# Kernel optimization log

Hardware: AMD Instinct MI355X
Metric: run time of the kernel (lower is better)

## Reference

```python
import jax, jax.numpy as jnp
import numpy as np

B, T, MED, LAB, GLU, D = 1024, 25, 145, 1956, 16, 64
H = D // 2  # 32


def _gat(h, adj, w, a):
    # h: [B, MED, 1] drug-usage counts; in_features=1 so Wh = h * w
    Wh = h * w  # [B, MED, D]
    f1 = Wh @ a[:D]  # [B, MED]
    f2 = Wh @ a[D:]  # [B, MED]
    e = jax.nn.leaky_relu(f1[:, :, None] + f2[:, None, :], 0.2)  # [B, MED, MED]
    e = jnp.where(adj > 0, e, jnp.float32(-9e15))
    attn = jax.nn.softmax(e, axis=-1)
    return jax.nn.elu(attn @ Wh)  # [B, MED, D]


def _mha(q, k, v, wq, wk, wv, wo, nh=4):
    Bq, Lq, Dm = q.shape
    dh = Dm // nh
    qh = (q @ wq).reshape(Bq, Lq, nh, dh)
    kh = (k @ wk).reshape(Bq, k.shape[1], nh, dh)
    vh = (v @ wv).reshape(Bq, v.shape[1], nh, dh)
    s = jnp.einsum('bqhd,bkhd->bhqk', qh, kh) / np.float32(np.sqrt(dh))
    a = jax.nn.softmax(s, axis=-1)
    o = jnp.einsum('bhqk,bkhd->bqhd', a, vh).reshape(Bq, Lq, Dm)
    return o @ wo


def _gated(x, g):
    # Attn_encoder: per-position gated emphasis, preserves sequence shape
    return x * jax.nn.sigmoid(x @ g)[..., None]


def setup_inputs():
    key = jax.random.key(0)
    ks = jax.random.split(key, 40)
    n = lambda i, shape, s=0.05: (jax.random.normal(ks[i], shape, dtype=jnp.float32) * s)
    inp = {
        'lab': jax.random.normal(ks[0], (B, LAB), dtype=jnp.float32),
        'glu': jax.random.normal(ks[1], (B, T, GLU), dtype=jnp.float32),
        'time_feat': jax.random.uniform(ks[2], (B, T, GLU), dtype=jnp.float32),
        'med': jax.random.uniform(ks[3], (B, T, MED), dtype=jnp.float32),
        'ehr_adj': (jax.random.uniform(ks[4], (MED, MED)) > 0.9).astype(jnp.float32),
        'ddi_adj': (jax.random.uniform(ks[5], (MED, MED)) > 0.9).astype(jnp.float32),
        'time_adj': (jax.random.uniform(ks[6], (MED, MED)) > 0.9).astype(jnp.float32),
        'sll_w1': n(7, (LAB, D)), 'sll_b1': n(8, (D,)),
        'sll_w2': n(9, (D, H)), 'sll_b2': n(10, (H,)),
        'glu_w': n(11, (2 * GLU, H)), 'glu_b': n(12, (H,)), 'glu_gate': n(13, (H,)),
        'med_w': n(14, (MED, D)), 'med_b': n(15, (D,)), 'med_gate': n(16, (D,)),
        'gat_ehr_w': n(17, (D,)), 'gat_ehr_a': n(18, (2 * D,)),
        'gat_time_w': n(19, (D,)), 'gat_time_a': n(20, (2 * D,)),
        'gat_ddi_w': n(21, (D,)), 'gat_ddi_a': n(22, (2 * D,)),
        'ga_wq': n(23, (D, D)), 'ga_wk': n(24, (D, D)), 'ga_wv': n(25, (D, D)), 'ga_wo': n(26, (D, D)),
        'm1_wq': n(27, (D, D)), 'm1_wk': n(28, (D, D)), 'm1_wv': n(29, (D, D)), 'm1_wo': n(30, (D, D)),
        'm2_wq': n(31, (D, D)), 'm2_wk': n(32, (D, D)), 'm2_wv': n(33, (D, D)), 'm2_wo': n(34, (D, D)),
        'out_w1': n(35, (MED * D, MED * D // 8), 0.01), 'out_b1': n(36, (MED * D // 8,)),
        'out_w2': n(37, (MED * D // 8, MED)), 'out_b2': n(38, (MED,)),
    }
    return inp


def reference(lab, glu, time_feat, med, ehr_adj, ddi_adj, time_adj,
              sll_w1, sll_b1, sll_w2, sll_b2,
              glu_w, glu_b, glu_gate, med_w, med_b, med_gate,
              gat_ehr_w, gat_ehr_a, gat_time_w, gat_time_a, gat_ddi_w, gat_ddi_a,
              ga_wq, ga_wk, ga_wv, ga_wo,
              m1_wq, m1_wk, m1_wv, m1_wo,
              m2_wq, m2_wk, m2_wv, m2_wo,
              out_w1, out_b1, out_w2, out_b2):
    relu = jax.nn.relu
    medb = (med > 0.9).astype(med.dtype)  # multi-hot medication history
    # static_ll, repeated over visits
    static = relu(relu(lab @ sll_w1 + sll_b1) @ sll_w2 + sll_b2)  # [B, H]
    static_seq = jnp.broadcast_to(static[:, None, :], (B, T, H))
    # per-patient drug usage counts over past visits
    h = jnp.sum(medb[:, :-1], axis=1)[..., None]  # [B, MED, 1]
    g_ehr = _gat(h, ehr_adj, gat_ehr_w, gat_ehr_a)
    g_time = _gat(h, time_adj, gat_time_w, gat_time_a)
    g_ddi = _gat(h, ddi_adj, gat_ddi_w, gat_ddi_a)
    all_graph = jnp.concatenate([g_ehr, g_time, g_ddi], axis=1)  # [B, 3*MED, D]
    dm = _mha(all_graph, all_graph, all_graph, ga_wq, ga_wk, ga_wv, ga_wo)
    drug_mem = dm.reshape(B, 3, MED, D).mean(axis=1)  # [B, MED, D]
    # medication / glucose encoders
    med_rep = _gated(medb[:, :-1] @ med_w + med_b, med_gate)  # [B, T-1, D]
    glu_in = jnp.concatenate([glu, time_feat], axis=-1)  # [B, T, 2*GLU]
    glu_rep = _gated(jnp.tanh(glu_in @ glu_w + glu_b), glu_gate)  # [B, T, H]
    patient = jnp.concatenate([glu_rep, static_seq], axis=-1)  # [B, T, D]
    # m1: query = med history, keys/values = patient visits
    E_en = _mha(med_rep, patient, patient, m1_wq, m1_wk, m1_wv, m1_wo)  # [B, T-1, D]
    e0 = E_en[:, :1]  # [B, 1, D]
    # m2: query = drug memory, keys/values = encoded state
    E_de = _mha(drug_mem, e0, e0, m2_wq, m2_wk, m2_wv, m2_wo)  # [B, MED, D]
    final = E_de.reshape(B, MED * D)
    hid = relu(relu(final) @ out_w1 + out_b1)
    return hid @ out_w2 + out_b2  # [B, MED]
```

## Files before the change

### kernel.cpp

```cpp
#include <hip/hip_runtime.h>
#include <math.h>

#define B_   1024
#define T_   25
#define MED_ 145
#define LAB_ 1956
#define GLU_ 16
#define D_   64
#define H_   32
#define HID_ 1160
#define KC_  978
#define OUTN_ (B_ * MED_)

__global__ __launch_bounds__(512) void k_pre(
    const float* __restrict__ lab, const float* __restrict__ sw1,
    const float* __restrict__ out_w1,
    const float* __restrict__ wo, const float* __restrict__ m2wv,
    const float* __restrict__ m2wo,
    float* __restrict__ part, float* __restrict__ w1c, float* __restrict__ W3) {
  __shared__ float smem[11920];
  const int tid = threadIdx.x;
  const int bid = blockIdx.x;
  if (bid < 256) {
    const int b0 = (bid >> 1) * 8;
    const int kc = bid & 1;
    const int k0 = kc * KC_;
    float* lab_f = smem;
    float* red   = smem + 7824;
    for (int e = tid; e < 8 * 489; e += 512) {
      int r = e / 489, i = e - r * 489;
      float2 v = ((const float2*)(lab + (size_t)(b0 + r) * LAB_ + k0))[i];
      lab_f[r * 978 + 2 * i] = v.x;
      lab_f[r * 978 + 2 * i + 1] = v.y;
    }
    __syncthreads();
    const int col = tid & 63;
    const int slice = tid >> 6;
    float acc[8] = {0.f, 0.f, 0.f, 0.f, 0.f, 0.f, 0.f, 0.f};
    #pragma unroll 2
    for (int k = slice; k < KC_; k += 8) {
      float w = sw1[(size_t)(k0 + k) * D_ + col];
      #pragma unroll
      for (int r = 0; r < 8; ++r) acc[r] = fmaf(lab_f[r * 978 + k], w, acc[r]);
    }
    __syncthreads();
    #pragma unroll
    for (int r = 0; r < 8; ++r) red[(r * 8 + slice) * 64 + col] = acc[r];
    __syncthreads();
    {
      int r = tid >> 6, d = tid & 63;
      float v = 0.f;
      #pragma unroll
      for (int s2 = 0; s2 < 8; ++s2) v += red[(r * 8 + s2) * 64 + d];
      part[(size_t)kc * B_ * D_ + (size_t)(b0 + r) * D_ + d] = v;
    }
  } else if (bid < 401) {
    const int idx = (bid - 256) * 512 + tid;
    const float* p = out_w1 + idx;
    float s = 0.f;
    #pragma unroll 8
    for (int m = 0; m < MED_; ++m) s += p[(size_t)m * D_ * HID_];
    w1c[idx] = s;
  } else {
    float* tmp = smem;
    for (int e = tid; e < 4096; e += 512) {
      int i = e >> 6, j = e & 63;
      float s = 0.f;
      #pragma unroll 8
      for (int k = 0; k < 64; ++k) s = fmaf(wo[i * 64 + k], m2wv[k * 64 + j], s);
      tmp[e] = s;
    }
    __syncthreads();
    for (int e = tid; e < 4096; e += 512) {
      int i = e >> 6, j = e & 63;
      float s = 0.f;
      #pragma unroll 8
      for (int k = 0; k < 64; ++k) s = fmaf(tmp[i * 64 + k], m2wo[k * 64 + j], s);
      W3[e] = s;
    }
  }
}

__global__ __launch_bounds__(256) void k_perb(
    const float* __restrict__ glu, const float* __restrict__ tf,
    const float* __restrict__ med, const float* __restrict__ part,
    const float* __restrict__ sb1, const float* __restrict__ sw2,
    const float* __restrict__ sb2,
    const float* __restrict__ glu_w, const float* __restrict__ glu_b,
    const float* __restrict__ glu_gate, const float* __restrict__ med_w,
    const float* __restrict__ med_b, const float* __restrict__ med_gate,
    const float* __restrict__ wq, const float* __restrict__ wk,
    const float* __restrict__ wv, const float* __restrict__ W3,
    float* __restrict__ rr) {
  const int b = blockIdx.x;
  const int tid = threadIdx.x;
  const int d = tid & 63;
  const int s4 = tid >> 6;
  __shared__ float xin_s[T_][2 * GLU_];
  __shared__ float y_s[T_][H_];
  __shared__ float gate_s[T_];
  __shared__ float medrow_s[160];
  __shared__ float t1_s[D_];
  __shared__ float st_s[H_];
  __shared__ float pat_s[28][D_];
  __shared__ float q0_s[D_];
  __shared__ float kh_s[T_][D_];
  __shared__ float vh_s[T_][D_];
  __shared__ float at_s[4][T_];
  __shared__ float o_s[D_];
  __shared__ float vec_s[D_];
  __shared__ float red4[4][D_];

  for (int e = tid; e < T_ * GLU_; e += 256) {
    int t = e >> 4, i = e & 15;
    xin_s[t][i] = glu[((size_t)b * T_ + t) * GLU_ + i];
    xin_s[t][GLU_ + i] = tf[((size_t)b * T_ + t) * GLU_ + i];
  }
  if (tid < MED_) medrow_s[tid] = med[(size_t)b * T_ * MED_ + tid];
  if (tid >= 192) {
    int dd = tid - 192;
    size_t o = (size_t)b * D_ + dd;
    t1_s[dd] = fmaxf(part[o] + part[(size_t)B_ * D_ + o] + sb1[dd], 0.f);
  }
  __syncthreads();

  for (int e = tid; e < T_ * H_; e += 256) {
    int t = e >> 5, j = e & 31;
    float s = glu_b[j];
    #pragma unroll 8
    for (int i = 0; i < 2 * GLU_; ++i) s = fmaf(xin_s[t][i], glu_w[i * H_ + j], s);
    y_s[t][j] = tanhf(s);
  }
  if (tid >= 224) {
    int j = tid - 224;
    float s = sb2[j];
    #pragma unroll 8
    for (int dd = 0; dd < D_; ++dd) s = fmaf(t1_s[dd], sw2[dd * H_ + j], s);
    st_s[j] = fmaxf(s, 0.f);
  }
  __syncthreads();

  {
    float x = 0.f;
    for (int m = s4; m < MED_; m += 4)
      if (medrow_s[m] > 0.9f) x += med_w[m * D_ + d];
    red4[s4][d] = x;
  }
  if (tid < 8 * T_) {
    int t = tid >> 3, sl = tid & 7;
    float s = 0.f;
    #pragma unroll
    for (int i = 0; i < 4; ++i) {
      int j = sl * 4 + i;
      s = fmaf(y_s[t][j], glu_gate[j], s);
    }
    s += __shfl_xor(s, 1);
    s += __shfl_xor(s, 2);
    s += __shfl_xor(s, 4);
    if (sl == 0) gate_s[t] = 1.f / (1.f + __expf(-s));
  }
  __syncthreads();

  if (tid < D_) {
    float x = med_b[tid] + red4[0][tid] + red4[1][tid] + red4[2][tid] + red4[3][tid];
    float v = x * med_gate[tid];
    #pragma unroll
    for (int off = 32; off > 0; off >>= 1) v += __shfl_xor(v, off);
    q0_s[tid] = x * (1.f / (1.f + __expf(-v)));
  }
  for (int e = tid; e < 28 * H_; e += 256) {
    int t = e >> 5, j = e & 31;
    if (t < T_) {
      pat_s[t][j] = y_s[t][j] * gate_s[t];
      pat_s[t][H_ + j] = st_s[j];
    } else {
      pat_s[t][j] = 0.f;
      pat_s[t][H_ + j] = 0.f;
    }
  }
  __syncthreads();

  {
    float aK[7] = {0.f, 0.f, 0.f, 0.f, 0.f, 0.f, 0.f};
    float aV[7] = {0.f, 0.f, 0.f, 0.f, 0.f, 0.f, 0.f};
    #pragma unroll 4
    for (int j = 0; j < D_; ++j) {
      float wkj = wk[j * D_ + d];
      float wvj = wv[j * D_ + d];
      #pragma unroll
      for (int i = 0; i < 7; ++i) {
        float p = pat_s[s4 + 4 * i][j];
        aK[i] = fmaf(p, wkj, aK[i]);
        aV[i] = fmaf(p, wvj, aV[i]);
      }
    }
    #pragma unroll
    for (int i = 0; i < 7; ++i) {
      int t = s4 + 4 * i;
      if (t < T_) { kh_s[t][d] = aK[i]; vh_s[t][d] = aV[i]; }
    }
  }
  {
    float qp = 0.f;
    #pragma unroll
    for (int i = 0; i < 16; ++i) {
      int j = s4 * 16 + i;
      qp = fmaf(q0_s[j], wq[j * D_ + d], qp);
    }
    red4[s4][d] = qp;
  }
  __syncthreads();

  if (tid < D_) vec_s[tid] = red4[0][tid] + red4[1][tid] + red4[2][tid] + red4[3][tid];
  __syncthreads();

  if (tid < 128) {
    int h = tid >> 5, t = tid & 31;
    bool valid = t < T_;
    float sc = -3.4e38f;
    if (valid) {
      float a = 0.f;
      #pragma unroll
      for (int i = 0; i < 16; ++i) a = fmaf(vec_s[h * 16 + i], kh_s[t][h * 16 + i], a);
      sc = a * 0.25f;
    }
    float m = sc;
    #pragma unroll
    for (int off = 16; off > 0; off >>= 1) m = fmaxf(m, __shfl_xor(m, off, 32));
    float e = valid ? __expf(sc - m) : 0.f;
    float sum = e;
    #pragma unroll
    for (int off = 16; off > 0; off >>= 1) sum += __shfl_xor(sum, off, 32);
    if (valid) at_s[h][t] = e / sum;
  }
  __syncthreads();

  if (tid < D_) {
    int h = tid >> 4;
    float s = 0.f;
    #pragma unroll
    for (int t = 0; t < T_; ++t) s = fmaf(at_s[h][t], vh_s[t][tid], s);
    o_s[tid] = s;
  }
  __syncthreads();

  {
    float p = 0.f;
    #pragma unroll
    for (int i = 0; i < 16; ++i) {
      int j = s4 * 16 + i;
      p = fmaf(o_s[j], W3[j * D_ + d], p);
    }
    red4[s4][d] = p;
  }
  __syncthreads();

  if (tid < D_) {
    float v = red4[0][tid] + red4[1][tid] + red4[2][tid] + red4[3][tid];
    rr[(size_t)b * D_ + tid] = fmaxf(v, 0.f);
  }
}

__global__ __launch_bounds__(640) void k_final(
    const float* __restrict__ rr, const float* __restrict__ w1c,
    const float* __restrict__ b1, const float* __restrict__ w2,
    float* __restrict__ p4) {
  const int tid = threadIdx.x;
  const int b0 = blockIdx.x * 16;
  const int jq = blockIdx.y;
  const int j0 = jq * 290;
  __shared__ float rr_s[16][D_];
  __shared__ float hid_s[16][292];
  for (int e = tid; e < 16 * D_; e += 640)
    ((float*)rr_s)[e] = rr[(size_t)b0 * D_ + e];
  __syncthreads();
  if (tid < 580) {
    int jj = tid % 290, rh = tid / 290;
    const float* wp = w1c + (size_t)(j0 + jj);
    float bb = b1[j0 + jj];
    float acc[8] = {0.f, 0.f, 0.f, 0.f, 0.f, 0.f, 0.f, 0.f};
    #pragma unroll 4
    for (int d4 = 0; d4 < 16; ++d4) {
      float w0 = wp[(size_t)(4 * d4 + 0) * HID_];
      float w1v = wp[(size_t)(4 * d4 + 1) * HID_];
      float w2v = wp[(size_t)(4 * d4 + 2) * HID_];
      float w3v = wp[(size_t)(4 * d4 + 3) * HID_];
      #pragma unroll
      for (int r8 = 0; r8 < 8; ++r8) {
        float4 rv = *(const float4*)&rr_s[rh * 8 + r8][4 * d4];
        acc[r8] += rv.x * w0 + rv.y * w1v + rv.z * w2v + rv.w * w3v;
      }
    }
    #pragma unroll
    for (int r8 = 0; r8 < 8; ++r8)
      hid_s[rh * 8 + r8][jj] = fmaxf(acc[r8] + bb, 0.f);
  }
  __syncthreads();
  if (tid < 580) {
    int n = tid % MED_, rg = tid / MED_;
    const float* w2p = w2 + (size_t)j0 * MED_ + n;
    float s0 = 0.f, s1 = 0.f, s2 = 0.f, s3 = 0.f;
    #pragma unroll 4
    for (int jv = 0; jv < 72; ++jv) {
      float wa = w2p[(size_t)(4 * jv + 0) * MED_];
      float wb = w2p[(size_t)(4 * jv + 1) * MED_];
      float wc = w2p[(size_t)(4 * jv + 2) * MED_];
      float wd = w2p[(size_t)(4 * jv + 3) * MED_];
      float4 h0 = *(const float4*)&hid_s[rg * 4 + 0][4 * jv];
      float4 h1 = *(const float4*)&hid_s[rg * 4 + 1][4 * jv];
      float4 h2 = *(const float4*)&hid_s[rg * 4 + 2][4 * jv];
      float4 h3 = *(const float4*)&hid_s[rg * 4 + 3][4 * jv];
      s0 += h0.x * wa + h0.y * wb + h0.z * wc + h0.w * wd;
      s1 += h1.x * wa + h1.y * wb + h1.z * wc + h1.w * wd;
      s2 += h2.x * wa + h2.y * wb + h2.z * wc + h2.w * wd;
      s3 += h3.x * wa + h3.y * wb + h3.z * wc + h3.w * wd;
    }
    {
      float wa = w2p[(size_t)288 * MED_];
      float wb = w2p[(size_t)289 * MED_];
      s0 += hid_s[rg * 4 + 0][288] * wa + hid_s[rg * 4 + 0][289] * wb;
      s1 += hid_s[rg * 4 + 1][288] * wa + hid_s[rg * 4 + 1][289] * wb;
      s2 += hid_s[rg * 4 + 2][288] * wa + hid_s[rg * 4 + 2][289] * wb;
      s3 += hid_s[rg * 4 + 3][288] * wa + hid_s[rg * 4 + 3][289] * wb;
    }
    float* dst = p4 + (size_t)jq * OUTN_;
    dst[(size_t)(b0 + rg * 4 + 0) * MED_ + n] = s0;
    dst[(size_t)(b0 + rg * 4 + 1) * MED_ + n] = s1;
    dst[(size_t)(b0 + rg * 4 + 2) * MED_ + n] = s2;
    dst[(size_t)(b0 + rg * 4 + 3) * MED_ + n] = s3;
  }
}

__global__ __launch_bounds__(256) void k_combine(
    const float* __restrict__ p4, const float* __restrict__ b2,
    float* __restrict__ out) {
  int idx = blockIdx.x * 256 + threadIdx.x;
  int n = idx - (idx / MED_) * MED_;
  out[idx] = p4[idx] + p4[OUTN_ + idx] + p4[2 * OUTN_ + idx] +
             p4[3 * OUTN_ + idx] + b2[n];
}

extern "C" void kernel_launch(void* const* d_in, const int* in_sizes, int n_in,
                              void* d_out, int out_size, void* d_ws, size_t ws_size,
                              hipStream_t stream) {
  (void)in_sizes; (void)n_in; (void)out_size; (void)ws_size;
  const float* lab      = (const float*)d_in[0];
  const float* glu      = (const float*)d_in[1];
  const float* tf       = (const float*)d_in[2];
  const float* med      = (const float*)d_in[3];
  const float* sll_w1   = (const float*)d_in[7];
  const float* sll_b1   = (const float*)d_in[8];
  const float* sll_w2   = (const float*)d_in[9];
  const float* sll_b2   = (const float*)d_in[10];
  const float* glu_w    = (const float*)d_in[11];
  const float* glu_b    = (const float*)d_in[12];
  const float* glu_gate = (const float*)d_in[13];
  const float* med_w    = (const float*)d_in[14];
  const float* med_b    = (const float*)d_in[15];
  const float* med_gate = (const float*)d_in[16];
  const float* m1_wq    = (const float*)d_in[27];
  const float* m1_wk    = (const float*)d_in[28];
  const float* m1_wv    = (const float*)d_in[29];
  const float* m1_wo    = (const float*)d_in[30];
  const float* m2_wv    = (const float*)d_in[33];
  const float* m2_wo    = (const float*)d_in[34];
  const float* out_w1   = (const float*)d_in[35];
  const float* out_b1   = (const float*)d_in[36];
  const float* out_w2   = (const float*)d_in[37];
  const float* out_b2   = (const float*)d_in[38];
  float* out = (float*)d_out;

  float* ws   = (float*)d_ws;
  float* part = ws;
  float* w1c  = part + 2 * B_ * D_;
  float* rr   = w1c + D_ * HID_;
  float* W3   = rr + B_ * D_;
  float* p4   = W3 + D_ * D_;

  hipLaunchKernelGGL(k_pre, dim3(402), dim3(512), 0, stream,
                     lab, sll_w1, out_w1, m1_wo, m2_wv, m2_wo, part, w1c, W3);
  hipLaunchKernelGGL(k_perb, dim3(B_), dim3(256), 0, stream,
                     glu, tf, med, part, sll_b1, sll_w2, sll_b2,
                     glu_w, glu_b, glu_gate, med_w, med_b, med_gate,
                     m1_wq, m1_wk, m1_wv, W3, rr);
  hipLaunchKernelGGL(k_final, dim3(B_ / 16, 4), dim3(640), 0, stream,
                     rr, w1c, out_b1, out_w2, p4);
  hipLaunchKernelGGL(k_combine, dim3(OUTN_ / 256), dim3(256), 0, stream,
                     p4, out_b2, out);
}
```

Measured before the change: 249.4 us.

## Split out_w1 column reduction across more blocks and rework final w2 GEMV mapping

The w1c reduction over 145 medication rows was done by 145 blocks, each thread serially summing all rows. It is now spread over 580 blocks, with four thread slices per column reducing through shared memory, to raise memory-level parallelism on a bandwidth-bound pass. The shared buffer is shrunk by reusing the lab tile for the reduction scratch. The final hidden-to-output GEMV in k_final now gives each thread one batch row and five adjacent outputs, replacing four rows per output column. This changes the w2 access pattern and the register pressure.

```diff
diff --git a/kernel.cpp b/kernel.cpp
--- a/kernel.cpp
+++ b/kernel.cpp
@@ -11,6 +11,7 @@
 #define HID_ 1160
 #define KC_  978
 #define OUTN_ (B_ * MED_)
+#define W1N_ (D_ * HID_)
 
 __global__ __launch_bounds__(512) void k_pre(
     const float* __restrict__ lab, const float* __restrict__ sw1,
@@ -18,7 +19,7 @@
     const float* __restrict__ wo, const float* __restrict__ m2wv,
     const float* __restrict__ m2wo,
     float* __restrict__ part, float* __restrict__ w1c, float* __restrict__ W3) {
-  __shared__ float smem[11920];
+  __shared__ float smem[7824];
   const int tid = threadIdx.x;
   const int bid = blockIdx.x;
   if (bid < 256) {
@@ -26,7 +27,6 @@
     const int kc = bid & 1;
     const int k0 = kc * KC_;
     float* lab_f = smem;
-    float* red   = smem + 7824;
     for (int e = tid; e < 8 * 489; e += 512) {
       int r = e / 489, i = e - r * 489;
       float2 v = ((const float2*)(lab + (size_t)(b0 + r) * LAB_ + k0))[i];
@@ -44,6 +44,7 @@
       for (int r = 0; r < 8; ++r) acc[r] = fmaf(lab_f[r * 978 + k], w, acc[r]);
     }
     __syncthreads();
+    float* red = smem;
     #pragma unroll
     for (int r = 0; r < 8; ++r) red[(r * 8 + slice) * 64 + col] = acc[r];
     __syncthreads();
@@ -54,13 +55,24 @@
       for (int s2 = 0; s2 < 8; ++s2) v += red[(r * 8 + s2) * 64 + d];
       part[(size_t)kc * B_ * D_ + (size_t)(b0 + r) * D_ + d] = v;
     }
-  } else if (bid < 401) {
-    const int idx = (bid - 256) * 512 + tid;
-    const float* p = out_w1 + idx;
+  } else if (bid < 836) {
+    const int b2 = bid - 256;
+    const int i = tid & 127;
+    const int msl = tid >> 7;
+    const int idx = b2 * 128 + i;
+    const int m0 = (msl * MED_) >> 2, m1 = ((msl + 1) * MED_) >> 2;
+    const float* p = out_w1 + idx + (size_t)m0 * W1N_;
     float s = 0.f;
-    #pragma unroll 8
-    for (int m = 0; m < MED_; ++m) s += p[(size_t)m * D_ * HID_];
-    w1c[idx] = s;
+    #pragma unroll 4
+    for (int m = m0; m < m1; ++m) {
+      s += *p;
+      p += (size_t)W1N_;
+    }
+    float* red = smem;
+    red[msl * 128 + i] = s;
+    __syncthreads();
+    if (tid < 128)
+      w1c[b2 * 128 + tid] = red[tid] + red[128 + tid] + red[256 + tid] + red[384 + tid];
   } else {
     float* tmp = smem;
     for (int e = tid; e < 4096; e += 512) {
@@ -296,38 +308,23 @@
       hid_s[rh * 8 + r8][jj] = fmaxf(acc[r8] + bb, 0.f);
   }
   __syncthreads();
-  if (tid < 580) {
-    int n = tid % MED_, rg = tid / MED_;
-    const float* w2p = w2 + (size_t)j0 * MED_ + n;
-    float s0 = 0.f, s1 = 0.f, s2 = 0.f, s3 = 0.f;
-    #pragma unroll 4
-    for (int jv = 0; jv < 72; ++jv) {
-      float wa = w2p[(size_t)(4 * jv + 0) * MED_];
-      float wb = w2p[(size_t)(4 * jv + 1) * MED_];
-      float wc = w2p[(size_t)(4 * jv + 2) * MED_];
-      float wd = w2p[(size_t)(4 * jv + 3) * MED_];
-      float4 h0 = *(const float4*)&hid_s[rg * 4 + 0][4 * jv];
-      float4 h1 = *(const float4*)&hid_s[rg * 4 + 1][4 * jv];
-      float4 h2 = *(const float4*)&hid_s[rg * 4 + 2][4 * jv];
-      float4 h3 = *(const float4*)&hid_s[rg * 4 + 3][4 * jv];
-      s0 += h0.x * wa + h0.y * wb + h0.z * wc + h0.w * wd;
-      s1 += h1.x * wa + h1.y * wb + h1.z * wc + h1.w * wd;
-      s2 += h2.x * wa + h2.y * wb + h2.z * wc + h2.w * wd;
-      s3 += h3.x * wa + h3.y * wb + h3.z * wc + h3.w * wd;
-    }
-    {
-      float wa = w2p[(size_t)288 * MED_];
-      float wb = w2p[(size_t)289 * MED_];
-      s0 += hid_s[rg * 4 + 0][288] * wa + hid_s[rg * 4 + 0][289] * wb;
-      s1 += hid_s[rg * 4 + 1][288] * wa + hid_s[rg * 4 + 1][289] * wb;
-      s2 += hid_s[rg * 4 + 2][288] * wa + hid_s[rg * 4 + 2][289] * wb;
-      s3 += hid_s[rg * 4 + 3][288] * wa + hid_s[rg * 4 + 3][289] * wb;
-    }
-    float* dst = p4 + (size_t)jq * OUTN_;
-    dst[(size_t)(b0 + rg * 4 + 0) * MED_ + n] = s0;
-    dst[(size_t)(b0 + rg * 4 + 1) * MED_ + n] = s1;
-    dst[(size_t)(b0 + rg * 4 + 2) * MED_ + n] = s2;
-    dst[(size_t)(b0 + rg * 4 + 3) * MED_ + n] = s3;
+  if (tid < 464) {
+    int ng = tid >> 4;
+    int r  = tid & 15;
+    const float* w2p = w2 + (size_t)j0 * MED_ + ng * 5;
+    float a0 = 0.f, a1 = 0.f, a2 = 0.f, a3 = 0.f, a4 = 0.f;
+    #pragma unroll 2
+    for (int k = 0; k < 290; ++k) {
+      float h = hid_s[r][k];
+      const float* wkp = w2p + (size_t)k * MED_;
+      a0 = fmaf(h, wkp[0], a0);
+      a1 = fmaf(h, wkp[1], a1);
+      a2 = fmaf(h, wkp[2], a2);
+      a3 = fmaf(h, wkp[3], a3);
+      a4 = fmaf(h, wkp[4], a4);
+    }
+    float* dst = p4 + (size_t)jq * OUTN_ + (size_t)(b0 + r) * MED_ + ng * 5;
+    dst[0] = a0; dst[1] = a1; dst[2] = a2; dst[3] = a3; dst[4] = a4;
   }
 }
 
@@ -373,11 +370,11 @@
   float* ws   = (float*)d_ws;
   float* part = ws;
   float* w1c  = part + 2 * B_ * D_;
-  float* rr   = w1c + D_ * HID_;
+  float* rr   = w1c + W1N_;
   float* W3   = rr + B_ * D_;
   float* p4   = W3 + D_ * D_;
 
-  hipLaunchKernelGGL(k_pre, dim3(402), dim3(512), 0, stream,
+  hipLaunchKernelGGL(k_pre, dim3(837), dim3(512), 0, stream,
                      lab, sll_w1, out_w1, m1_wo, m2_wv, m2_wo, part, w1c, W3);
   hipLaunchKernelGGL(k_perb, dim3(B_), dim3(256), 0, stream,
                      glu, tf, med, part, sll_b1, sll_w2, sll_b2,
```

After: 289.6 us. +16.2%, slower.
